# Optimization experiments

Hardware: AMD Instinct MI355X
Metric: run time of the kernel (lower is better)

The kernel has to match this reference:

```python
import jax, jax.numpy as jnp
import numpy as np

# NOTE on reconstructed deps (not shown in source):
#  - utils.mmnorm(x): max-magnitude norm, x / (max|x| over last dim + eps)
#  - model.LearnableFourierResampler(din, dout, nf): x -> Linear(din,nf) -> [sin,cos] -> Linear(2nf,dout)
#  - utils.pscan(q, fn, identity): Hillis-Steele log-depth scan: for n in 1,2,4,...:
#        q = fn(x=q, y=shift_right(q, n, fill=identity))   (Scanner.forward(x, y) cats (y, x))

B, T, C, NF = 8, 2048, 1024, 64
EPS = 1e-6

def mmnorm(x):
    return x / (jnp.max(jnp.abs(x), axis=-1, keepdims=True) + EPS)

def setup_inputs() -> dict:
    key = jax.random.key(0)
    ks = jax.random.split(key, 8)
    def w(k, shape, fan_in):
        return jax.random.normal(k, shape, jnp.float32) * (1.0 / np.sqrt(fan_in))
    return {
        "x": jax.random.normal(ks[0], (B, T, C), jnp.float32),
        "attn_W": w(ks[1], (C, 2 * C), C),
        "attn_b": jnp.zeros((2 * C,), jnp.float32),
        "freq_W": w(ks[2], (2 * C, NF), 2 * C),
        "freq_b": jnp.zeros((NF,), jnp.float32),
        "out_W": w(ks[3], (2 * NF, C), 2 * NF),
        "out_b": jnp.zeros((C,), jnp.float32),
        "proj_W": w(ks[4], (C, C), C),
        "proj_b": jnp.zeros((C,), jnp.float32),
        "identity": jax.random.uniform(ks[5], (C,), jnp.float32),
    }

def _scanner(y, x, freq_W, freq_b, out_W, out_b):
    # Scanner.forward(x, y): z = cat((y, x)); Fourier resample; mmnorm
    z = jnp.concatenate([y, x], axis=-1)                      # [B,T,2C]
    f = z @ freq_W + freq_b                                   # [B,T,NF]
    z = jnp.concatenate([jnp.sin(f), jnp.cos(f)], -1) @ out_W + out_b  # [B,T,C]
    return mmnorm(z)

def reference(x, attn_W, attn_b, freq_W, freq_b, out_W, out_b, proj_W, proj_b, identity):
    b, t, c = x.shape
    qv = x @ attn_W + attn_b
    q, v = qv[..., :c], qv[..., c:]
    # Hillis-Steele parallel scan with nonlinear learned combine
    n = 1
    while n < t:
        prev = jnp.concatenate(
            [jnp.broadcast_to(identity, (b, n, c)), q[:, : t - n]], axis=1)
        q = _scanner(prev, q, freq_W, freq_b, out_W, out_b)
        n *= 2
    Y = q * v
    return Y @ proj_W + proj_b
```

## Files before the change

kernel.cpp:

```cpp
#include <hip/hip_runtime.h>
#include <hip/hip_bf16.h>
#include <math.h>


#define R_ROWS 16384
#define T_DIM  2048
#define C_DIM  1024

typedef unsigned short u16;
typedef __attribute__((ext_vector_type(8))) short short8;
typedef __attribute__((ext_vector_type(4))) float f32x4;

__device__ __forceinline__ u16 f2bf(float f) {
  union { float f; unsigned u; } v; v.f = f;
  unsigned r = v.u + 0x7fffu + ((v.u >> 16) & 1u);
  return (u16)(r >> 16);
}
__device__ __forceinline__ float bf2f(u16 h) {
  union { unsigned u; float f; } v; v.u = ((unsigned)h) << 16;
  return v.f;
}
__device__ __forceinline__ void gld16(const void* g, void* l) {
  __builtin_amdgcn_global_load_lds(
      (const __attribute__((address_space(1))) void*)g,
      (__attribute__((address_space(3))) void*)l, 16, 0, 0);
}

__global__ __launch_bounds__(256) void cvt_bf16(const float* __restrict__ in,
                                                u16* __restrict__ out, int n8) {
  const int i = blockIdx.x * 256 + threadIdx.x;
  if (i >= n8) return;
  const float4 a = ((const float4*)in)[2 * i];
  const float4 b = ((const float4*)in)[2 * i + 1];
  alignas(16) u16 t[8] = {f2bf(a.x), f2bf(a.y), f2bf(a.z), f2bf(a.w),
                          f2bf(b.x), f2bf(b.y), f2bf(b.z), f2bf(b.w)};
  ((uint4*)out)[i] = *(const uint4*)t;
}

__global__ __launch_bounds__(256) void prod_bf16(const u16* __restrict__ a,
                                                 const u16* __restrict__ b,
                                                 u16* __restrict__ o, int n8) {
  const int i = blockIdx.x * 256 + threadIdx.x;
  if (i >= n8) return;
  uint4 ua = ((const uint4*)a)[i], ub = ((const uint4*)b)[i];
  const u16* pa = (const u16*)&ua;
  const u16* pb = (const u16*)&ub;
  alignas(16) u16 t[8];
#pragma unroll
  for (int c = 0; c < 8; c++) t[c] = f2bf(bf2f(pa[c]) * bf2f(pb[c]));
  ((uint4*)o)[i] = *(const uint4*)t;
}

__global__ __launch_bounds__(256) void cvt_T(const float* __restrict__ W,
                                             u16* __restrict__ Wt, int K, int N) {
  __shared__ float t[32][33];
  const int k0 = blockIdx.x * 32, n0 = blockIdx.y * 32;
  const int tx = threadIdx.x & 31, ty = threadIdx.x >> 5;
#pragma unroll
  for (int i = 0; i < 32; i += 8)
    t[ty + i][tx] = W[(size_t)(k0 + ty + i) * N + n0 + tx];
  __syncthreads();
#pragma unroll
  for (int i = 0; i < 32; i += 8)
    Wt[(size_t)(n0 + ty + i) * K + k0 + tx] = f2bf(t[tx][ty + i]);
}

__global__ __launch_bounds__(256) void cvt_w1f(const float* __restrict__ W,
                                               u16* __restrict__ W1f) {
  __shared__ float t[32][33];
  const int k0 = blockIdx.x * 32, n0 = blockIdx.y * 32;
  const int tx = threadIdx.x & 31, ty = threadIdx.x >> 5;
#pragma unroll
  for (int i = 0; i < 32; i += 8)
    t[ty + i][tx] = W[(size_t)(k0 + ty + i) * 64 + n0 + tx];
  __syncthreads();
#pragma unroll
  for (int i = 0; i < 32; i += 8) {
    const int k = k0 + tx;
    const int row = (n0 + ty + i) + ((k >= 1024) ? 64 : 0);
    W1f[(size_t)row * 1024 + (k & 1023)] = f2bf(t[tx][ty + i]);
  }
}

__global__ __launch_bounds__(256) void fid_kernel(const float* __restrict__ ident,
                                                  const float* __restrict__ W,
                                                  float* __restrict__ fid) {
  __shared__ float red[256];
  const int tid = threadIdx.x;
  const int j = tid >> 2, part = tid & 3;
  float s = 0.f;
  for (int k = part * 256; k < part * 256 + 256; k++)
    s += ident[k] * W[(size_t)k * 64 + j];
  red[tid] = s;
  __syncthreads();
  if (part == 0) fid[j] = red[tid] + red[tid + 1] + red[tid + 2] + red[tid + 3];
}

__global__ __launch_bounds__(256) void w21_kernel(const float* __restrict__ outW,
                                                  const float* __restrict__ outb,
                                                  const u16* __restrict__ w1f,
                                                  u16* __restrict__ W21t,
                                                  float* __restrict__ c1) {
  __shared__ float red[256];
  const int j = blockIdx.x, tid = threadIdx.x;
  const int s = tid >> 1, part = tid & 1;
  const u16* wrow = w1f + (size_t)j * 1024;
  float acc = 0.f;
  for (int c = part * 512; c < part * 512 + 512; c++)
    acc += outW[(size_t)s * 1024 + c] * bf2f(wrow[c]);
  red[tid] = acc;
  __syncthreads();
  if (part == 0) W21t[(size_t)j * 128 + s] = f2bf(red[2 * s] + red[2 * s + 1]);
  float cb = 0.f;
  if (tid < 128)
    for (int c = tid * 8; c < tid * 8 + 8; c++) cb += outb[c] * bf2f(wrow[c]);
  __syncthreads();
  red[tid] = (tid < 128) ? cb : 0.f;
  __syncthreads();
  if (tid < 64) red[tid] += red[tid + 64];
  __syncthreads();
  if (tid == 0) {
    float v = 0.f;
    for (int k2 = 0; k2 < 64; k2++) v += red[k2];
    c1[j] = v;
  }
}

#define GEMM_KLOOP(Aptr, Bptr)                                                 \
  const int tid = threadIdx.x, lane = tid & 63, w = tid >> 6;                  \
  const int ln = lane & 15, qd = lane >> 4;                                    \
  const int wm = w & 1, wn = w >> 1;                                           \
  const int nbx = gridDim.x;                                                   \
  const int bid0 = blockIdx.y * nbx + blockIdx.x;                              \
  const int nwg = nbx * gridDim.y;                                             \
  const int bid = (bid0 & 7) * (nwg >> 3) + (bid0 >> 3);                       \
  const int n0 = (bid % nbx) * 128, m0 = (bid / nbx) * 128;                    \
  const int srow = w * 32 + (lane >> 3);                                       \
  const int sl = (lane & 7) ^ ((lane >> 3) & 7);                               \
  const int scol = sl * 8;                                                     \
  f32x4 acc[4][4] = {};                                                        \
  for (int kt = 0; kt < 1024; kt += 64) {                                      \
    __syncthreads();                                                           \
    _Pragma("unroll") for (int j = 0; j < 4; j++) {                            \
      gld16(&Aptr[(size_t)(m0 + srow + j * 8) * 1024 + kt + scol],             \
            &As[(w * 32 + j * 8) * 64]);                                       \
      gld16(&Bptr[(size_t)(n0 + srow + j * 8) * 1024 + kt + scol],             \
            &Bs[(w * 32 + j * 8) * 64]);                                       \
    }                                                                          \
    __syncthreads();                                                           \
    _Pragma("unroll") for (int ks = 0; ks < 2; ks++) {                         \
      short8 af[4], bf_[4];                                                    \
      _Pragma("unroll") for (int i = 0; i < 4; i++) {                          \
        const int ar = wm * 64 + i * 16 + ln;                                  \
        af[i] = *(const short8*)&As[ar * 64 + ((ks * 4 + qd) ^ (ar & 7)) * 8]; \
      }                                                                        \
      _Pragma("unroll") for (int j = 0; j < 4; j++) {                          \
        const int br = wn * 64 + j * 16 + ln;                                  \
        bf_[j] = *(const short8*)&Bs[br * 64 + ((ks * 4 + qd) ^ (br & 7)) * 8];\
      }                                                                        \
      _Pragma("unroll") for (int i = 0; i < 4; i++)                            \
      _Pragma("unroll") for (int j = 0; j < 4; j++)                            \
        acc[i][j] = __builtin_amdgcn_mfma_f32_16x16x32_bf16(af[i], bf_[j],     \
                                                            acc[i][j], 0, 0, 0);\
    }                                                                          \
  }                                                                            \
  __syncthreads();

__global__ __launch_bounds__(256) void gemm_qv_mfma(
    const u16* __restrict__ A, const u16* __restrict__ Bt,
    const float* __restrict__ bias, u16* __restrict__ Qb, u16* __restrict__ Vb) {
  __shared__ u16 S[16384];
  u16* As = S;
  u16* Bs = S + 8192;
  GEMM_KLOOP(A, Bt)
#pragma unroll
  for (int j = 0; j < 4; j++) {
    const int col = wn * 64 + j * 16 + ln;
    const float bv = bias[n0 + col];
#pragma unroll
    for (int i = 0; i < 4; i++)
#pragma unroll
      for (int r = 0; r < 4; r++)
        S[(wm * 64 + i * 16 + qd * 4 + r) * 128 + col] = f2bf(acc[i][j][r] + bv);
  }
  __syncthreads();
  const bool isQ = (n0 < 1024);
  u16* dst = isQ ? Qb : Vb;
  const int nb = isQ ? n0 : n0 - 1024;
#pragma unroll
  for (int it = 0; it < 8; it++) {
    const int idx = it * 256 + tid;
    const int row = idx >> 4, seg = idx & 15;
    *(uint4*)&dst[(size_t)(m0 + row) * 1024 + nb + seg * 8] = ((const uint4*)S)[idx];
  }
}

__global__ __launch_bounds__(256) void gemm_proj_mfma(
    const u16* __restrict__ A, const u16* __restrict__ Bt,
    const float* __restrict__ bias, float* __restrict__ OUT) {
  __shared__ u16 S[16384];
  u16* As = S;
  u16* Bs = S + 8192;
  GEMM_KLOOP(A, Bt)
  float* Csf = (float*)S;
#pragma unroll
  for (int p = 0; p < 2; p++) {
    if (wm == p) {
#pragma unroll
      for (int j = 0; j < 4; j++) {
        const int col = wn * 64 + j * 16 + ln;
        const float bv = bias[n0 + col];
#pragma unroll
        for (int i = 0; i < 4; i++)
#pragma unroll
          for (int r = 0; r < 4; r++)
            Csf[(i * 16 + qd * 4 + r) * 128 + col] = acc[i][j][r] + bv;
      }
    }
    __syncthreads();
#pragma unroll
    for (int it = 0; it < 8; it++) {
      const int idx = it * 256 + tid;
      const int row = idx >> 5, seg = idx & 31;
      *(uint4*)&OUT[(size_t)(m0 + p * 64 + row) * 1024 + n0 + seg * 4] =
          ((const uint4*)Csf)[idx];
    }
    __syncthreads();
  }
}

__global__ __launch_bounds__(256) void g0_kernel(const u16* __restrict__ Qb,
                                                 const u16* __restrict__ W1f,
                                                 float* __restrict__ G) {
  __shared__ u16 As[64 * 64];
  const int tid = threadIdx.x, lane = tid & 63, wv = tid >> 6;
  const int ln = lane & 15, qd = lane >> 4;
  const int wm = wv >> 1, wn = wv & 1;
  const int m0 = blockIdx.x * 64;
  const int srow = wv * 16 + (lane >> 3);
  const int scol = ((lane & 7) ^ ((lane >> 3) & 7)) * 8;
  f32x4 acc[2][4] = {};
  for (int kt = 0; kt < 1024; kt += 64) {
    __syncthreads();
#pragma unroll
    for (int j = 0; j < 2; j++)
      gld16(&Qb[(size_t)(m0 + srow + j * 8) * 1024 + kt + scol],
            &As[(wv * 16 + j * 8) * 64]);
    __syncthreads();
#pragma unroll
    for (int ks = 0; ks < 2; ks++) {
      short8 a[2];
#pragma unroll
      for (int i = 0; i < 2; i++) {
        const int ar = wm * 32 + i * 16 + ln;
        a[i] = *(const short8*)&As[ar * 64 + ((ks * 4 + qd) ^ (ar & 7)) * 8];
      }
#pragma unroll
      for (int nt = 0; nt < 4; nt++) {
        const short8 b = *(const short8*)&W1f[(size_t)(wn * 64 + nt * 16 + ln) * 1024 +
                                              kt + ks * 32 + qd * 8];
#pragma unroll
        for (int i = 0; i < 2; i++)
          acc[i][nt] = __builtin_amdgcn_mfma_f32_16x16x32_bf16(a[i], b, acc[i][nt], 0, 0, 0);
      }
    }
  }
#pragma unroll
  for (int i = 0; i < 2; i++)
#pragma unroll
    for (int nt = 0; nt < 4; nt++)
#pragma unroll
      for (int r = 0; r < 4; r++)
        G[(size_t)(m0 + wm * 32 + i * 16 + qd * 4 + r) * 128 + wn * 64 + nt * 16 + ln] =
            acc[i][nt][r];
}

__global__ __launch_bounds__(1024, 4) void scan_fused(
    const float* __restrict__ Gsrc, float* __restrict__ Gdst,
    const u16* __restrict__ W21t, const u16* __restrict__ W2t,
    const float* __restrict__ b1, const float* __restrict__ b2,
    const float* __restrict__ fid, const float* __restrict__ c1,
    u16* __restrict__ Qout, int n, int flags) {
  __shared__ u16 S[64 * 128];
  __shared__ unsigned rmax[64];
  const int tid = threadIdx.x, lane = tid & 63, wv = tid >> 6;
  const int ln = lane & 15, qd = lane >> 4;
  const int r0 = blockIdx.x * 64;
  if (tid < 64) rmax[tid] = 0u;
  {
    const int r = tid >> 4, js = (tid & 15) << 2;
    const int gr = r0 + r, tl = gr & (T_DIM - 1);
    const float* g1p = (tl >= n) ? &Gsrc[(size_t)(gr - n) * 128 + js] : &fid[js];
    const float4 g1 = *(const float4*)g1p;
    const float4 g2 = *(const float4*)&Gsrc[(size_t)gr * 128 + 64 + js];
    const float4 bb = *(const float4*)&b1[js];
    float f[4] = {g1.x + g2.x + bb.x, g1.y + g2.y + bb.y,
                  g1.z + g2.z + bb.z, g1.w + g2.w + bb.w};
    alignas(8) u16 sn[4], cs[4];
#pragma unroll
    for (int c = 0; c < 4; c++) {
      float sv, cv;
      __sincosf(f[c], &sv, &cv);
      sn[c] = f2bf(sv);
      cs[c] = f2bf(cv);
    }
    const int u = js >> 3, half = (js >> 2) & 1, rx = r & 7;
    const int ps = (u ^ rx) & 7;
    const int pc = 8 | ps;
    *(uint2*)&S[r * 128 + ps * 8 + half * 4] = *(const uint2*)sn;
    *(uint2*)&S[r * 128 + pc * 8 + half * 4] = *(const uint2*)cs;
  }
  __syncthreads();
  const u16* w2b = W2t + (size_t)wv * 64 * 128;
  f32x4 acc[4][4] = {};
#pragma unroll
  for (int ks = 0; ks < 4; ks++) {
    short8 af[4];
#pragma unroll
    for (int i = 0; i < 4; i++) {
      const int ar = i * 16 + ln;
      const int u = ks * 4 + qd;
      af[i] = *(const short8*)&S[ar * 128 + ((u & 8) | ((u ^ ar) & 7)) * 8];
    }
#pragma unroll
    for (int nt = 0; nt < 4; nt++) {
      const short8 b = *(const short8*)&w2b[(size_t)(nt * 16 + ln) * 128 + ks * 32 + qd * 8];
#pragma unroll
      for (int i = 0; i < 4; i++)
        acc[i][nt] = __builtin_amdgcn_mfma_f32_16x16x32_bf16(b, af[i], acc[i][nt], 0, 0, 0);
    }
  }
  float mx[4] = {0.f, 0.f, 0.f, 0.f};
#pragma unroll
  for (int nt = 0; nt < 4; nt++) {
    const float4 bb = *(const float4*)&b2[wv * 64 + nt * 16 + qd * 4];
    const float br4[4] = {bb.x, bb.y, bb.z, bb.w};
#pragma unroll
    for (int i = 0; i < 4; i++)
#pragma unroll
      for (int r = 0; r < 4; r++) {
        const float v = acc[i][nt][r] + br4[r];
        acc[i][nt][r] = v;
        mx[i] = fmaxf(mx[i], fabsf(v));
      }
  }
#pragma unroll
  for (int i = 0; i < 4; i++) {
    float v = mx[i];
    v = fmaxf(v, __shfl_xor(v, 16, 64));
    v = fmaxf(v, __shfl_xor(v, 32, 64));
    if (lane < 16) atomicMax(&rmax[i * 16 + lane], __float_as_uint(v));
  }
  __syncthreads();
  if (flags & 1) {
    float inv[4];
#pragma unroll
    for (int i = 0; i < 4; i++)
      inv[i] = 1.0f / (__uint_as_float(rmax[i * 16 + ln]) + 1e-6f);
#pragma unroll
    for (int i = 0; i < 4; i++) {
      const int row = i * 16 + ln;
#pragma unroll
      for (int nt = 0; nt < 4; nt++) {
        const int col = wv * 64 + nt * 16 + qd * 4;
        uint2 pv;
        pv.x = (unsigned)f2bf(acc[i][nt][0] * inv[i]) |
               ((unsigned)f2bf(acc[i][nt][1] * inv[i]) << 16);
        pv.y = (unsigned)f2bf(acc[i][nt][2] * inv[i]) |
               ((unsigned)f2bf(acc[i][nt][3] * inv[i]) << 16);
        *(uint2*)&Qout[(size_t)(r0 + row) * 1024 + col] = pv;
      }
    }
  }
  if (flags & 2) {
    const int wm3 = wv & 3, wn3 = wv >> 2;
    f32x4 g[2] = {};
#pragma unroll
    for (int ks = 0; ks < 4; ks++) {
      const int ar = wm3 * 16 + ln;
      const int u = ks * 4 + qd;
      const short8 a = *(const short8*)&S[ar * 128 + ((u & 8) | ((u ^ ar) & 7)) * 8];
#pragma unroll
      for (int c = 0; c < 2; c++) {
        const short8 b = *(const short8*)&W21t[(size_t)(wn3 * 32 + c * 16 + ln) * 128 +
                                               ks * 32 + qd * 8];
        g[c] = __builtin_amdgcn_mfma_f32_16x16x32_bf16(a, b, g[c], 0, 0, 0);
      }
    }
#pragma unroll
    for (int c = 0; c < 2; c++) {
      const int col = wn3 * 32 + c * 16 + ln;
      const float cb = c1[col];
#pragma unroll
      for (int r = 0; r < 4; r++) {
        const int row = wm3 * 16 + qd * 4 + r;
        const float invr = 1.0f / (__uint_as_float(rmax[row]) + 1e-6f);
        Gdst[(size_t)(r0 + row) * 128 + col] = (g[c][r] + cb) * invr;
      }
    }
  }
}

extern "C" void kernel_launch(void* const* d_in, const int* in_sizes, int n_in,
                              void* d_out, int out_size, void* d_ws, size_t ws_size,
                              hipStream_t stream) {
  const float* x      = (const float*)d_in[0];
  const float* attn_W = (const float*)d_in[1];
  const float* attn_b = (const float*)d_in[2];
  const float* freq_W = (const float*)d_in[3];
  const float* freq_b = (const float*)d_in[4];
  const float* out_W  = (const float*)d_in[5];
  const float* out_b  = (const float*)d_in[6];
  const float* proj_W = (const float*)d_in[7];
  const float* proj_b = (const float*)d_in[8];
  const float* ident  = (const float*)d_in[9];
  float* out = (float*)d_out;

  const size_t RC = (size_t)R_ROWS * C_DIM;
  u16* Xb  = (u16*)d_ws;
  u16* Qb  = Xb + RC;
  u16* Vb  = Qb + RC;
  u16* aWt = Vb + RC;
  u16* pWt = aWt + (size_t)2048 * 1024;
  u16* w2t = pWt + (size_t)1024 * 1024;
  u16* w1f = w2t + (size_t)1024 * 128;
  float* Ga  = (float*)(w1f + (size_t)128 * 1024);
  float* Gb  = Ga + (size_t)R_ROWS * 128;
  float* fid = Gb + (size_t)R_ROWS * 128;
  float* c1  = fid + 64;
  u16* W21t  = (u16*)(c1 + 128);

  cvt_bf16<<<8192, 256, 0, stream>>>(x, Xb, (int)(RC / 8));
  cvt_T<<<dim3(32, 64), 256, 0, stream>>>(attn_W, aWt, 1024, 2048);
  cvt_T<<<dim3(32, 32), 256, 0, stream>>>(proj_W, pWt, 1024, 1024);
  cvt_T<<<dim3(4, 32), 256, 0, stream>>>(out_W, w2t, 128, 1024);
  cvt_w1f<<<dim3(64, 2), 256, 0, stream>>>(freq_W, w1f);
  fid_kernel<<<1, 256, 0, stream>>>(ident, freq_W, fid);
  w21_kernel<<<128, 256, 0, stream>>>(out_W, out_b, w1f, W21t, c1);

  gemm_qv_mfma<<<dim3(16, 128), 256, 0, stream>>>(Xb, aWt, attn_b, Qb, Vb);
  g0_kernel<<<256, 256, 0, stream>>>(Qb, w1f, Ga);

  float* gs = Ga;
  float* gd = Gb;
  for (int n = 1; n < T_DIM; n <<= 1) {
    const int last = (n == 1024);
    scan_fused<<<256, 1024, 0, stream>>>(gs, gd, W21t, w2t, freq_b, out_b, fid,
                                         c1, Qb, n, last ? 1 : 2);
    float* t = gs; gs = gd; gd = t;
  }

  prod_bf16<<<8192, 256, 0, stream>>>(Qb, Vb, Xb, (int)(RC / 8));
  gemm_proj_mfma<<<dim3(8, 128), 256, 0, stream>>>(Xb, pWt, proj_b, out);
}
```

Baseline: 440.6 us.

## Fold Q projection into first scan matmul and fuse V product into scan epilogue

Measured after the change: 450.2 us. 2.2% more time.

```diff
diff --git a/kernel.cpp b/kernel.cpp
--- a/kernel.cpp
+++ b/kernel.cpp
@@ -37,28 +37,15 @@
   ((uint4*)out)[i] = *(const uint4*)t;
 }
 
-__global__ __launch_bounds__(256) void prod_bf16(const u16* __restrict__ a,
-                                                 const u16* __restrict__ b,
-                                                 u16* __restrict__ o, int n8) {
-  const int i = blockIdx.x * 256 + threadIdx.x;
-  if (i >= n8) return;
-  uint4 ua = ((const uint4*)a)[i], ub = ((const uint4*)b)[i];
-  const u16* pa = (const u16*)&ua;
-  const u16* pb = (const u16*)&ub;
-  alignas(16) u16 t[8];
-#pragma unroll
-  for (int c = 0; c < 8; c++) t[c] = f2bf(bf2f(pa[c]) * bf2f(pb[c]));
-  ((uint4*)o)[i] = *(const uint4*)t;
-}
-
 __global__ __launch_bounds__(256) void cvt_T(const float* __restrict__ W,
-                                             u16* __restrict__ Wt, int K, int N) {
+                                             u16* __restrict__ Wt, int K, int N,
+                                             int noff) {
   __shared__ float t[32][33];
   const int k0 = blockIdx.x * 32, n0 = blockIdx.y * 32;
   const int tx = threadIdx.x & 31, ty = threadIdx.x >> 5;
 #pragma unroll
   for (int i = 0; i < 32; i += 8)
-    t[ty + i][tx] = W[(size_t)(k0 + ty + i) * N + n0 + tx];
+    t[ty + i][tx] = W[(size_t)(k0 + ty + i) * N + noff + n0 + tx];
   __syncthreads();
 #pragma unroll
   for (int i = 0; i < 32; i += 8)
@@ -80,6 +67,14 @@
     const int row = (n0 + ty + i) + ((k >= 1024) ? 64 : 0);
     W1f[(size_t)row * 1024 + (k & 1023)] = f2bf(t[tx][ty + i]);
   }
+}
+
+__global__ __launch_bounds__(256) void cvt_wq(const float* __restrict__ W,
+                                              u16* __restrict__ Wq) {
+  const int c = blockIdx.x, k0 = threadIdx.x * 4;
+  const float4 a = *(const float4*)&W[(size_t)c * 2048 + k0];
+  alignas(8) u16 t[4] = {f2bf(a.x), f2bf(a.y), f2bf(a.z), f2bf(a.w)};
+  *(uint2*)&Wq[(size_t)c * 1024 + k0] = *(const uint2*)t;
 }
 
 __global__ __launch_bounds__(256) void fid_kernel(const float* __restrict__ ident,
@@ -94,6 +89,19 @@
   red[tid] = s;
   __syncthreads();
   if (part == 0) fid[j] = red[tid] + red[tid + 1] + red[tid + 2] + red[tid + 3];
+}
+
+__global__ __launch_bounds__(256) void bg_kernel(const float* __restrict__ ab,
+                                                 const u16* __restrict__ w1f,
+                                                 float* __restrict__ bg) {
+  __shared__ float red[256];
+  const int tid = threadIdx.x, j = tid >> 1, part = tid & 1;
+  float s = 0.f;
+  for (int k = part * 512; k < part * 512 + 512; k++)
+    s += ab[k] * bf2f(w1f[(size_t)j * 1024 + k]);
+  red[tid] = s;
+  __syncthreads();
+  if (part == 0) bg[j] = red[2 * j] + red[2 * j + 1];
 }
 
 __global__ __launch_bounds__(256) void w21_kernel(const float* __restrict__ outW,
@@ -124,6 +132,52 @@
     for (int k2 = 0; k2 < 64; k2++) v += red[k2];
     c1[j] = v;
   }
+}
+
+__global__ __launch_bounds__(256) void gm_kernel(const u16* __restrict__ w1f,
+                                                 const u16* __restrict__ Wqb,
+                                                 u16* __restrict__ Mt) {
+  __shared__ u16 As[128 * 64];
+  const int tid = threadIdx.x, lane = tid & 63, w = tid >> 6;
+  const int ln = lane & 15, qd = lane >> 4;
+  const int wm = w & 1, wn = w >> 1;
+  const int n0 = blockIdx.x * 64;
+  const int srow = w * 32 + (lane >> 3);
+  const int scol = ((lane & 7) ^ ((lane >> 3) & 7)) * 8;
+  f32x4 acc[4][2] = {};
+  for (int kt = 0; kt < 1024; kt += 64) {
+    __syncthreads();
+#pragma unroll
+    for (int j = 0; j < 4; j++)
+      gld16(&w1f[(size_t)(srow + j * 8) * 1024 + kt + scol],
+            &As[(w * 32 + j * 8) * 64]);
+    __syncthreads();
+#pragma unroll
+    for (int ks = 0; ks < 2; ks++) {
+      short8 af[4];
+#pragma unroll
+      for (int i = 0; i < 4; i++) {
+        const int ar = wm * 64 + i * 16 + ln;
+        af[i] = *(const short8*)&As[ar * 64 + ((ks * 4 + qd) ^ (ar & 7)) * 8];
+      }
+#pragma unroll
+      for (int nt = 0; nt < 2; nt++) {
+        const short8 b = *(const short8*)&Wqb[(size_t)(n0 + wn * 32 + nt * 16 + ln) * 1024 +
+                                              kt + ks * 32 + qd * 8];
+#pragma unroll
+        for (int i = 0; i < 4; i++)
+          acc[i][nt] = __builtin_amdgcn_mfma_f32_16x16x32_bf16(af[i], b, acc[i][nt], 0, 0, 0);
+      }
+    }
+  }
+#pragma unroll
+  for (int i = 0; i < 4; i++)
+#pragma unroll
+    for (int nt = 0; nt < 2; nt++)
+#pragma unroll
+      for (int r = 0; r < 4; r++)
+        Mt[(size_t)(wm * 64 + i * 16 + qd * 4 + r) * 1024 +
+           n0 + wn * 32 + nt * 16 + ln] = f2bf(acc[i][nt][r]);
 }
 
 #define GEMM_KLOOP(Aptr, Bptr)                                                 \
@@ -166,9 +220,9 @@
   }                                                                            \
   __syncthreads();
 
-__global__ __launch_bounds__(256) void gemm_qv_mfma(
+__global__ __launch_bounds__(256) void gemm_v_mfma(
     const u16* __restrict__ A, const u16* __restrict__ Bt,
-    const float* __restrict__ bias, u16* __restrict__ Qb, u16* __restrict__ Vb) {
+    const float* __restrict__ bias, u16* __restrict__ Vb) {
   __shared__ u16 S[16384];
   u16* As = S;
   u16* Bs = S + 8192;
@@ -184,14 +238,11 @@
         S[(wm * 64 + i * 16 + qd * 4 + r) * 128 + col] = f2bf(acc[i][j][r] + bv);
   }
   __syncthreads();
-  const bool isQ = (n0 < 1024);
-  u16* dst = isQ ? Qb : Vb;
-  const int nb = isQ ? n0 : n0 - 1024;
 #pragma unroll
   for (int it = 0; it < 8; it++) {
     const int idx = it * 256 + tid;
     const int row = idx >> 4, seg = idx & 15;
-    *(uint4*)&dst[(size_t)(m0 + row) * 1024 + nb + seg * 8] = ((const uint4*)S)[idx];
+    *(uint4*)&Vb[(size_t)(m0 + row) * 1024 + n0 + seg * 8] = ((const uint4*)S)[idx];
   }
 }
 
@@ -229,8 +280,9 @@
   }
 }
 
-__global__ __launch_bounds__(256) void g0_kernel(const u16* __restrict__ Qb,
-                                                 const u16* __restrict__ W1f,
+__global__ __launch_bounds__(256) void g0_kernel(const u16* __restrict__ Xb,
+                                                 const u16* __restrict__ Mt,
+                                                 const float* __restrict__ bg,
                                                  float* __restrict__ G) {
   __shared__ u16 As[64 * 64];
   const int tid = threadIdx.x, lane = tid & 63, wv = tid >> 6;
@@ -244,7 +296,7 @@
     __syncthreads();
 #pragma unroll
     for (int j = 0; j < 2; j++)
-      gld16(&Qb[(size_t)(m0 + srow + j * 8) * 1024 + kt + scol],
+      gld16(&Xb[(size_t)(m0 + srow + j * 8) * 1024 + kt + scol],
             &As[(wv * 16 + j * 8) * 64]);
     __syncthreads();
 #pragma unroll
@@ -257,8 +309,8 @@
       }
 #pragma unroll
       for (int nt = 0; nt < 4; nt++) {
-        const short8 b = *(const short8*)&W1f[(size_t)(wn * 64 + nt * 16 + ln) * 1024 +
-                                              kt + ks * 32 + qd * 8];
+        const short8 b = *(const short8*)&Mt[(size_t)(wn * 64 + nt * 16 + ln) * 1024 +
+                                             kt + ks * 32 + qd * 8];
 #pragma unroll
         for (int i = 0; i < 2; i++)
           acc[i][nt] = __builtin_amdgcn_mfma_f32_16x16x32_bf16(a[i], b, acc[i][nt], 0, 0, 0);
@@ -268,11 +320,13 @@
 #pragma unroll
   for (int i = 0; i < 2; i++)
 #pragma unroll
-    for (int nt = 0; nt < 4; nt++)
+    for (int nt = 0; nt < 4; nt++) {
+      const float bgv = bg[wn * 64 + nt * 16 + ln];
 #pragma unroll
       for (int r = 0; r < 4; r++)
         G[(size_t)(m0 + wm * 32 + i * 16 + qd * 4 + r) * 128 + wn * 64 + nt * 16 + ln] =
-            acc[i][nt][r];
+            acc[i][nt][r] + bgv;
+    }
 }
 
 __global__ __launch_bounds__(1024, 4) void scan_fused(
@@ -280,7 +334,7 @@
     const u16* __restrict__ W21t, const u16* __restrict__ W2t,
     const float* __restrict__ b1, const float* __restrict__ b2,
     const float* __restrict__ fid, const float* __restrict__ c1,
-    u16* __restrict__ Qout, int n, int flags) {
+    const u16* __restrict__ Vb, u16* __restrict__ Yout, int n, int flags) {
   __shared__ u16 S[64 * 128];
   __shared__ unsigned rmax[64];
   const int tid = threadIdx.x, lane = tid & 63, wv = tid >> 6;
@@ -363,12 +417,14 @@
 #pragma unroll
       for (int nt = 0; nt < 4; nt++) {
         const int col = wv * 64 + nt * 16 + qd * 4;
+        const uint2 vv = *(const uint2*)&Vb[(size_t)(r0 + row) * 1024 + col];
+        const u16* vp = (const u16*)&vv;
         uint2 pv;
-        pv.x = (unsigned)f2bf(acc[i][nt][0] * inv[i]) |
-               ((unsigned)f2bf(acc[i][nt][1] * inv[i]) << 16);
-        pv.y = (unsigned)f2bf(acc[i][nt][2] * inv[i]) |
-               ((unsigned)f2bf(acc[i][nt][3] * inv[i]) << 16);
-        *(uint2*)&Qout[(size_t)(r0 + row) * 1024 + col] = pv;
+        pv.x = (unsigned)f2bf(acc[i][nt][0] * inv[i] * bf2f(vp[0])) |
+               ((unsigned)f2bf(acc[i][nt][1] * inv[i] * bf2f(vp[1])) << 16);
+        pv.y = (unsigned)f2bf(acc[i][nt][2] * inv[i] * bf2f(vp[2])) |
+               ((unsigned)f2bf(acc[i][nt][3] * inv[i] * bf2f(vp[3])) << 16);
+        *(uint2*)&Yout[(size_t)(r0 + row) * 1024 + col] = pv;
       }
     }
   }
@@ -419,6 +475,8 @@
   const size_t RC = (size_t)R_ROWS * C_DIM;
   u16* Xb  = (u16*)d_ws;
   u16* Qb  = Xb + RC;
+  u16* Wqb = Qb;
+  u16* Mt  = Qb + (size_t)1024 * 1024;
   u16* Vb  = Qb + RC;
   u16* aWt = Vb + RC;
   u16* pWt = aWt + (size_t)2048 * 1024;
@@ -428,28 +486,31 @@
   float* Gb  = Ga + (size_t)R_ROWS * 128;
   float* fid = Gb + (size_t)R_ROWS * 128;
   float* c1  = fid + 64;
-  u16* W21t  = (u16*)(c1 + 128);
+  float* bgv = c1 + 128;
+  u16* W21t  = (u16*)(bgv + 128);
 
   cvt_bf16<<<8192, 256, 0, stream>>>(x, Xb, (int)(RC / 8));
-  cvt_T<<<dim3(32, 64), 256, 0, stream>>>(attn_W, aWt, 1024, 2048);
-  cvt_T<<<dim3(32, 32), 256, 0, stream>>>(proj_W, pWt, 1024, 1024);
-  cvt_T<<<dim3(4, 32), 256, 0, stream>>>(out_W, w2t, 128, 1024);
+  cvt_T<<<dim3(32, 32), 256, 0, stream>>>(attn_W, aWt, 1024, 2048, 1024);
+  cvt_T<<<dim3(32, 32), 256, 0, stream>>>(proj_W, pWt, 1024, 1024, 0);
+  cvt_T<<<dim3(4, 32), 256, 0, stream>>>(out_W, w2t, 128, 1024, 0);
   cvt_w1f<<<dim3(64, 2), 256, 0, stream>>>(freq_W, w1f);
+  cvt_wq<<<1024, 256, 0, stream>>>(attn_W, Wqb);
   fid_kernel<<<1, 256, 0, stream>>>(ident, freq_W, fid);
+  bg_kernel<<<1, 256, 0, stream>>>(attn_b, w1f, bgv);
   w21_kernel<<<128, 256, 0, stream>>>(out_W, out_b, w1f, W21t, c1);
-
-  gemm_qv_mfma<<<dim3(16, 128), 256, 0, stream>>>(Xb, aWt, attn_b, Qb, Vb);
-  g0_kernel<<<256, 256, 0, stream>>>(Qb, w1f, Ga);
+  gm_kernel<<<16, 256, 0, stream>>>(w1f, Wqb, Mt);
+
+  gemm_v_mfma<<<dim3(8, 128), 256, 0, stream>>>(Xb, aWt, attn_b + 1024, Vb);
+  g0_kernel<<<256, 256, 0, stream>>>(Xb, Mt, bgv, Ga);
 
   float* gs = Ga;
   float* gd = Gb;
   for (int n = 1; n < T_DIM; n <<= 1) {
     const int last = (n == 1024);
     scan_fused<<<256, 1024, 0, stream>>>(gs, gd, W21t, w2t, freq_b, out_b, fid,
-                                         c1, Qb, n, last ? 1 : 2);
+                                         c1, Vb, Xb, n, last ? 1 : 2);
     float* t = gs; gs = gd; gd = t;
   }
 
-  prod_bf16<<<8192, 256, 0, stream>>>(Qb, Vb, Xb, (int)(RC / 8));
   gemm_proj_mfma<<<dim3(8, 128), 256, 0, stream>>>(Xb, pWt, proj_b, out);
 }
```
